# Performance work log

Hardware: AMD Instinct MI355X
Metric: run time of the kernel (lower is better)

The kernel has to match this reference:

```python
import jax, jax.numpy as jnp
import numpy as np

MAX_SEQ_LENGTH = 32
LN_EPS = 1e-5


def setup_inputs() -> dict:
    key = jax.random.key(0)
    ks = jax.random.split(key, 6)
    N, T, D, H, O = 256, 1024, 128, 256, 128
    G = 4 * H
    # torch kaiming_normal_ on a 2D (in, 4H) tensor: fan_in = size(1) = 4H, std = sqrt(2/fan_in)
    std_k = float(np.sqrt(2.0 / G))
    X = jax.random.normal(ks[0], (N, T, D), dtype=jnp.float32)
    Wx = jax.random.normal(ks[1], (D, G), dtype=jnp.float32) * std_k
    Wh = jax.random.normal(ks[2], (H, G), dtype=jnp.float32) * std_k
    b = jnp.zeros((G,), dtype=jnp.float32)
    W1 = jax.random.normal(ks[3], (H, H), dtype=jnp.float32) * float(np.sqrt(1.0 / H))
    b1 = jnp.zeros((H,), dtype=jnp.float32)
    ln_gamma = jnp.ones((H,), dtype=jnp.float32)
    ln_beta = jnp.zeros((H,), dtype=jnp.float32)
    W2 = jax.random.normal(ks[4], (H, O), dtype=jnp.float32) * float(np.sqrt(1.0 / H))
    b2 = jnp.zeros((O,), dtype=jnp.float32)
    return {"X": X, "Wx": Wx, "Wh": Wh, "b": b, "W1": W1, "b1": b1,
            "ln_gamma": ln_gamma, "ln_beta": ln_beta, "W2": W2, "b2": b2}


def _fc(h, W1, b1, ln_gamma, ln_beta, W2, b2):
    z = h @ W1 + b1
    mu = jnp.mean(z, axis=-1, keepdims=True)
    var = jnp.var(z, axis=-1, keepdims=True)
    z = (z - mu) * jax.lax.rsqrt(var + LN_EPS) * ln_gamma + ln_beta
    z = jax.nn.relu(z)
    return z @ W2 + b2


def reference(X, Wx, Wh, b, W1, b1, ln_gamma, ln_beta, W2, b2):
    N, T, D = X.shape
    H = Wh.shape[0]
    h0 = jnp.zeros((N, H), dtype=X.dtype)
    c0 = jnp.zeros((N, H), dtype=X.dtype)

    # --- encoder: standard LSTM cell (sigmoid/tanh gates) ---
    def enc_step(carry, x_t):
        h, c = carry
        fm = x_t @ Wx + h @ Wh + b  # (N, 4H)
        i = jax.nn.sigmoid(fm[:, 0:H])
        f = jax.nn.sigmoid(fm[:, H:2 * H])
        o = jax.nn.sigmoid(fm[:, 2 * H:3 * H])
        g = jnp.tanh(fm[:, 3 * H:4 * H])
        c = c * f + i * g
        h = o * jnp.tanh(c)
        return (h, c), None

    (h, c), _ = jax.lax.scan(enc_step, (h0, c0), jnp.swapaxes(X, 0, 1))

    # --- decoder: NOTE original code uses RAW gate slices (no sigmoid/tanh),
    # and start_token is zeros so the start_token @ Wx term is exactly 0. ---
    def dec_step(carry, _):
        h, c = carry
        fm = h @ Wh + b  # zeros @ Wx contributes 0
        i = fm[:, 0:H]
        f = fm[:, H:2 * H]
        o = fm[:, 2 * H:3 * H]
        g = fm[:, 3 * H:4 * H]
        c = c * f + i * g
        h = o * jnp.tanh(c)
        y = _fc(h, W1, b1, ln_gamma, ln_beta, W2, b2)
        return (h, c), y

    _, ys = jax.lax.scan(dec_step, (h, c), None, length=MAX_SEQ_LENGTH)
    return jnp.swapaxes(ys, 0, 1)  # (N, max_seq_length, output_dim)
```

## Files before the change

kernel.cpp:

```cpp
#include <hip/hip_runtime.h>
#include <cmath>

typedef _Float16 f16;
typedef _Float16 f16x8v __attribute__((ext_vector_type(8)));
typedef float f32x4v __attribute__((ext_vector_type(4)));

#define NTHR 256
#define WPG  16

__device__ __forceinline__ float fexp2_(float x) {
#if __has_builtin(__builtin_amdgcn_exp2f)
  return __builtin_amdgcn_exp2f(x);
#else
  return exp2f(x);
#endif
}
__device__ __forceinline__ float frcp_(float x) {
#if __has_builtin(__builtin_amdgcn_rcpf)
  return __builtin_amdgcn_rcpf(x);
#else
  return 1.0f / x;
#endif
}
__device__ __forceinline__ float fsigmoid(float x) {
  float xc = fminf(fmaxf(x, -60.f), 60.f);
  return frcp_(1.f + fexp2_(xc * -1.44269504f));
}
__device__ __forceinline__ float ftanh_(float x) {
  float xc = fminf(fmaxf(x, -15.f), 15.f);
  float e = fexp2_(xc * 2.88539008f);
  return (e - 1.f) * frcp_(e + 1.f);
}

__device__ __forceinline__ void st_sc_u(unsigned* p, unsigned v) {
  asm volatile("global_store_dword %0, %1, off sc0 sc1" :: "v"(p), "v"(v) : "memory");
}
__device__ __forceinline__ void st_sc_f(float* p, float v) {
  asm volatile("global_store_dword %0, %1, off sc0 sc1" :: "v"(p), "v"(v) : "memory");
}

__device__ __forceinline__ void ld64u_sc(const unsigned* p, uint4& a, uint4& b,
                                         uint4& c, uint4& d) {
  asm volatile(
      "global_load_dwordx4 %0, %4, off sc0 sc1\n\t"
      "global_load_dwordx4 %1, %4, off offset:16 sc0 sc1\n\t"
      "global_load_dwordx4 %2, %4, off offset:32 sc0 sc1\n\t"
      "global_load_dwordx4 %3, %4, off offset:48 sc0 sc1\n\t"
      "s_waitcnt vmcnt(0)"
      : "=&v"(a), "=&v"(b), "=&v"(c), "=&v"(d) : "v"(p) : "memory");
}
__device__ __forceinline__ void ld4f_sc(const float* p, float4& a, float4& b,
                                        float4& c, float4& d) {
  asm volatile(
      "global_load_dwordx4 %0, %4, off sc0 sc1\n\t"
      "global_load_dwordx4 %1, %5, off sc0 sc1\n\t"
      "global_load_dwordx4 %2, %6, off sc0 sc1\n\t"
      "global_load_dwordx4 %3, %7, off sc0 sc1\n\t"
      "s_waitcnt vmcnt(0)"
      : "=&v"(a), "=&v"(b), "=&v"(c), "=&v"(d)
      : "v"(p), "v"(p + 1024), "v"(p + 2048), "v"(p + 3072) : "memory");
}

__device__ __forceinline__ void arrive_bar(unsigned* cg) {
  asm volatile("s_waitcnt vmcnt(0)" ::: "memory");
  __syncthreads();
  if (threadIdx.x == 0)
    (void)__hip_atomic_fetch_add(cg, 1u, __ATOMIC_RELAXED, __HIP_MEMORY_SCOPE_AGENT);
}
__device__ __forceinline__ void wait_bar(unsigned* cg, unsigned target) {
  if (threadIdx.x == 0) {
    unsigned guard = 0;
    while (__hip_atomic_load(cg, __ATOMIC_RELAXED, __HIP_MEMORY_SCOPE_AGENT) < target) {
      __builtin_amdgcn_s_sleep(1);
      if (++guard > (1u << 22)) break;
    }
  }
  __syncthreads();
}

__device__ __forceinline__ unsigned packhl(float v) {
  f16 h = (f16)v;
  f16 lo = (f16)(v - (float)h);
  unsigned short hb, lb;
  __builtin_memcpy(&hb, &h, 2); __builtin_memcpy(&lb, &lo, 2);
  return (unsigned)hb | ((unsigned)lb << 16);
}
__device__ __forceinline__ float unpackf(unsigned u) {
  unsigned short hb = (unsigned short)(u & 0xffffu), lb = (unsigned short)(u >> 16);
  f16 h, l;
  __builtin_memcpy(&h, &hb, 2); __builtin_memcpy(&l, &lb, 2);
  return (float)h + (float)l;
}
__device__ __forceinline__ void unpack_wr(uint4 c, f16* ph, f16* pl) {
  unsigned h01 = (c.x & 0xffffu) | (c.y << 16);
  unsigned h23 = (c.z & 0xffffu) | (c.w << 16);
  unsigned l01 = (c.x >> 16) | (c.y & 0xffff0000u);
  unsigned l23 = (c.z >> 16) | (c.w & 0xffff0000u);
  uint2 hh = {h01, h23}, ll = {l01, l23};
  *(uint2*)ph = hh; *(uint2*)pl = ll;
}
__device__ __forceinline__ void conv8_wr(float4 a, float4 b, f16* ph, f16* pl) {
  f16x8v h, l;
  h[0]=(f16)a.x; h[1]=(f16)a.y; h[2]=(f16)a.z; h[3]=(f16)a.w;
  h[4]=(f16)b.x; h[5]=(f16)b.y; h[6]=(f16)b.z; h[7]=(f16)b.w;
  l[0]=(f16)(a.x-(float)h[0]); l[1]=(f16)(a.y-(float)h[1]);
  l[2]=(f16)(a.z-(float)h[2]); l[3]=(f16)(a.w-(float)h[3]);
  l[4]=(f16)(b.x-(float)h[4]); l[5]=(f16)(b.y-(float)h[5]);
  l[6]=(f16)(b.z-(float)h[6]); l[7]=(f16)(b.w-(float)h[7]);
  *(f16x8v*)ph = h; *(f16x8v*)pl = l;
}

__global__ __launch_bounds__(NTHR, 1) void lstm_k(
    const float* __restrict__ X,  const float* __restrict__ Wx,
    const float* __restrict__ Wh, const float* __restrict__ Bg,
    const float* __restrict__ W1, const float* __restrict__ B1,
    const float* __restrict__ LNG, const float* __restrict__ LNB,
    const float* __restrict__ W2, const float* __restrict__ B2,
    float* __restrict__ Y, unsigned* __restrict__ CNT,
    unsigned* __restrict__ HBp, float* __restrict__ ZB)
{
  __shared__ f16   A_hi[16][392];
  __shared__ f16   A_lo[16][392];
  __shared__ float fm_w[4][16][20];
  __shared__ float hst[16][260];
  __shared__ float w1_lds[16][268];
  __shared__ float w2_lds[8][268];
  __shared__ float lng_lds[256], lnb_lds[256];
  __shared__ float ln_mu[16], ln_rs[16];

  const int tid = threadIdx.x;
  const int wg  = blockIdx.x;
  const int g   = wg & 15;
  const int jm  = wg >> 4;
  const int n0  = g * 16;
  const int k0  = jm * 16;
  unsigned* cg  = CNT + g * 32;

  const int l     = tid & 63;
  const int wv    = __builtin_amdgcn_readfirstlane(tid >> 6);
  const int arow  = l & 15;
  const int krow0 = (l >> 4) * 8;

  const int qq = (l >> 2) & 3;
  const int hc = l & 3;
  const int ch = k0 + 4 * wv + hc;

  f16x8v Bh[12], Bl[12];
  {
    const int bcol = qq * 256 + ch;
    #pragma unroll
    for (int kt = 0; kt < 12; ++kt) {
      #pragma unroll
      for (int j = 0; j < 8; ++j) {
        int k = kt * 32 + krow0 + j;
        float v = (kt < 4) ? Wx[k * 1024 + bcol] : Wh[(k - 128) * 1024 + bcol];
        f16 hi = (f16)v;
        Bh[kt][j] = hi;
        Bl[kt][j] = (f16)(v - (float)hi);
      }
    }
  }

  for (int idx = tid; idx < 256 * 16; idx += NTHR) {
    int k = idx >> 4, cc = idx & 15;
    w1_lds[cc][k] = W1[k * 256 + k0 + cc];
  }
  for (int idx = tid; idx < 256 * 8; idx += NTHR) {
    int k = idx >> 3, cc = idx & 7;
    w2_lds[cc][k] = W2[k * 128 + jm * 8 + cc];
  }
  lng_lds[tid] = LNG[tid];
  lnb_lds[tid] = LNB[tid];

  const float biasI = Bg[        ch];
  const float biasF = Bg[256   + ch];
  const float biasO = Bg[512   + ch];
  const float biasG = Bg[768   + ch];
  const int   myrow = (l >> 4) * 4 + qq;
  float c_reg = 0.0f;

  const int gr = tid >> 4, gk = tid & 15;
  const float b1reg = B1[k0 + gk];
  const float b2reg = (tid < 128) ? B2[jm * 8 + (tid & 7)] : 0.0f;

  {
    const float* xp = X + (size_t)(n0 + (tid >> 4)) * 131072 + (size_t)(tid & 15) * 8;
    conv8_wr(*(const float4*)xp, *(const float4*)(xp + 4),
             &A_hi[tid >> 4][(tid & 15) * 8], &A_lo[tid >> 4][(tid & 15) * 8]);
    f16x8v z8 = {0,0,0,0,0,0,0,0};
    *(f16x8v*)&A_hi[tid >> 4][128 + (tid & 15) * 16]     = z8;
    *(f16x8v*)&A_hi[tid >> 4][128 + (tid & 15) * 16 + 8] = z8;
    *(f16x8v*)&A_lo[tid >> 4][128 + (tid & 15) * 16]     = z8;
    *(f16x8v*)&A_lo[tid >> 4][128 + (tid & 15) * 16 + 8] = z8;
  }
  __syncthreads();

  auto stage_hA = [&](const unsigned* hb) {
    const int row = tid >> 4, cb = (tid & 15) * 16;
    uint4 c0, c1, c2, c3;
    ld64u_sc(hb + (size_t)row * 256 + cb, c0, c1, c2, c3);
    unpack_wr(c0, &A_hi[row][128 + cb],      &A_lo[row][128 + cb]);
    unpack_wr(c1, &A_hi[row][128 + cb + 4],  &A_lo[row][128 + cb + 4]);
    unpack_wr(c2, &A_hi[row][128 + cb + 8],  &A_lo[row][128 + cb + 8]);
    unpack_wr(c3, &A_hi[row][128 + cb + 12], &A_lo[row][128 + cb + 12]);
  };

  for (int t = 0; t < 1024; ++t) {
    float4 xa, xb;
    if (t < 1023) {
      const float* xp = X + (size_t)(n0 + (tid >> 4)) * 131072
                          + (size_t)(t + 1) * 128 + (size_t)(tid & 15) * 8;
      xa = *(const float4*)xp;
      xb = *(const float4*)(xp + 4);
    }

    f32x4v ac0 = {0,0,0,0}, ac1 = {0,0,0,0}, ac2 = {0,0,0,0};
    {
      f16x8v xh[4], xl[4];
      const f16* pah = &A_hi[arow][krow0];
      const f16* pal = &A_lo[arow][krow0];
      #pragma unroll
      for (int kt = 0; kt < 4; ++kt) {
        xh[kt] = *(const f16x8v*)(pah + kt * 32);
        xl[kt] = *(const f16x8v*)(pal + kt * 32);
      }
      #pragma unroll
      for (int kt = 0; kt < 4; ++kt) {
        ac0 = __builtin_amdgcn_mfma_f32_16x16x32_f16(xh[kt], Bh[kt], ac0, 0, 0, 0);
        ac1 = __builtin_amdgcn_mfma_f32_16x16x32_f16(xh[kt], Bl[kt], ac1, 0, 0, 0);
        ac2 = __builtin_amdgcn_mfma_f32_16x16x32_f16(xl[kt], Bh[kt], ac2, 0, 0, 0);
      }
    }

    if (t > 0) {
      wait_bar(cg, (unsigned)(WPG * t));
      stage_hA(HBp + (size_t)((t - 1) & 1) * 65536 + (size_t)n0 * 256);
      __syncthreads();
    }

    {
      f16x8v hh[8], hl[8];
      const f16* pah = &A_hi[arow][128 + krow0];
      const f16* pal = &A_lo[arow][128 + krow0];
      #pragma unroll
      for (int kt = 0; kt < 8; ++kt) {
        hh[kt] = *(const f16x8v*)(pah + kt * 32);
        hl[kt] = *(const f16x8v*)(pal + kt * 32);
      }
      #pragma unroll
      for (int kt = 0; kt < 8; ++kt) {
        ac0 = __builtin_amdgcn_mfma_f32_16x16x32_f16(hh[kt], Bh[kt + 4], ac0, 0, 0, 0);
        ac1 = __builtin_amdgcn_mfma_f32_16x16x32_f16(hh[kt], Bl[kt + 4], ac1, 0, 0, 0);
        ac2 = __builtin_amdgcn_mfma_f32_16x16x32_f16(hl[kt], Bh[kt + 4], ac2, 0, 0, 0);
      }
    }

    {
      f32x4v ac = ac0 + ac1 + ac2;
      *(f32x4v*)&fm_w[wv][l & 15][(l >> 4) * 4] = ac;
      float fi = fm_w[wv][     hc][myrow] + biasI;
      float ff = fm_w[wv][ 4 + hc][myrow] + biasF;
      float fo = fm_w[wv][ 8 + hc][myrow] + biasO;
      float fg = fm_w[wv][12 + hc][myrow] + biasG;
      float si = fsigmoid(fi), sf = fsigmoid(ff), so = fsigmoid(fo);
      float tg = ftanh_(fg);
      c_reg = c_reg * sf + si * tg;
      float hv = so * ftanh_(c_reg);
      st_sc_u(HBp + (size_t)(t & 1) * 65536 + (size_t)(n0 + myrow) * 256 + ch,
              packhl(hv));
    }

    if (t == 0) __syncthreads();
    if (t < 1023)
      conv8_wr(xa, xb, &A_hi[tid >> 4][(tid & 15) * 8], &A_lo[tid >> 4][(tid & 15) * 8]);
    arrive_bar(cg);
  }

  wait_bar(cg, (unsigned)(WPG * 1024));
  stage_hA(HBp + (size_t)65536 + (size_t)n0 * 256);
  __syncthreads();
  unsigned arr = 1024;

  for (int s = 0; s < 32; ++s) {
    const int t = 1024 + s;

    f32x4v ac0 = {0,0,0,0}, ac1 = {0,0,0,0}, ac2 = {0,0,0,0};
    {
      f16x8v hh[8], hl[8];
      const f16* pah = &A_hi[arow][128 + krow0];
      const f16* pal = &A_lo[arow][128 + krow0];
      #pragma unroll
      for (int kt = 0; kt < 8; ++kt) {
        hh[kt] = *(const f16x8v*)(pah + kt * 32);
        hl[kt] = *(const f16x8v*)(pal + kt * 32);
      }
      #pragma unroll
      for (int kt = 0; kt < 8; ++kt) {
        ac0 = __builtin_amdgcn_mfma_f32_16x16x32_f16(hh[kt], Bh[kt + 4], ac0, 0, 0, 0);
        ac1 = __builtin_amdgcn_mfma_f32_16x16x32_f16(hh[kt], Bl[kt + 4], ac1, 0, 0, 0);
        ac2 = __builtin_amdgcn_mfma_f32_16x16x32_f16(hl[kt], Bh[kt + 4], ac2, 0, 0, 0);
      }
    }
    {
      f32x4v ac = ac0 + ac1 + ac2;
      *(f32x4v*)&fm_w[wv][l & 15][(l >> 4) * 4] = ac;
      float fi = fm_w[wv][     hc][myrow] + biasI;
      float ff = fm_w[wv][ 4 + hc][myrow] + biasF;
      float fo = fm_w[wv][ 8 + hc][myrow] + biasO;
      float fg = fm_w[wv][12 + hc][myrow] + biasG;
      c_reg = c_reg * ff + fi * fg;
      float hv = fo * ftanh_(c_reg);
      st_sc_u(HBp + (size_t)(t & 1) * 65536 + (size_t)(n0 + myrow) * 256 + ch,
              packhl(hv));
    }
    arrive_bar(cg); ++arr;
    wait_bar(cg, WPG * arr);

    {
      const int row = tid >> 4, cb = (tid & 15) * 16;
      const unsigned* hb = HBp + (size_t)(t & 1) * 65536 + (size_t)n0 * 256
                               + (size_t)row * 256 + cb;
      uint4 c0, c1, c2, c3;
      ld64u_sc(hb, c0, c1, c2, c3);
      unpack_wr(c0, &A_hi[row][128 + cb],      &A_lo[row][128 + cb]);
      unpack_wr(c1, &A_hi[row][128 + cb + 4],  &A_lo[row][128 + cb + 4]);
      unpack_wr(c2, &A_hi[row][128 + cb + 8],  &A_lo[row][128 + cb + 8]);
      unpack_wr(c3, &A_hi[row][128 + cb + 12], &A_lo[row][128 + cb + 12]);
      float4 f0 = {unpackf(c0.x), unpackf(c0.y), unpackf(c0.z), unpackf(c0.w)};
      float4 f1 = {unpackf(c1.x), unpackf(c1.y), unpackf(c1.z), unpackf(c1.w)};
      float4 f2 = {unpackf(c2.x), unpackf(c2.y), unpackf(c2.z), unpackf(c2.w)};
      float4 f3 = {unpackf(c3.x), unpackf(c3.y), unpackf(c3.z), unpackf(c3.w)};
      *(float4*)&hst[row][cb]      = f0;
      *(float4*)&hst[row][cb + 4]  = f1;
      *(float4*)&hst[row][cb + 8]  = f2;
      *(float4*)&hst[row][cb + 12] = f3;
    }
    __syncthreads();

    {
      float za = b1reg;
      const float* hr = &hst[gr][0];
      const float* wr = &w1_lds[gk][0];
      #pragma unroll 4
      for (int kc = 0; kc < 64; ++kc) {
        float4 h4 = *(const float4*)(hr + kc * 4);
        float4 w4 = *(const float4*)(wr + kc * 4);
        za = fmaf(h4.x, w4.x, fmaf(h4.y, w4.y, fmaf(h4.z, w4.z, fmaf(h4.w, w4.w, za))));
      }
      st_sc_f(ZB + (size_t)(n0 + gr) * 256 + k0 + gk, za);
    }
    arrive_bar(cg); ++arr;
    wait_bar(cg, WPG * arr);

    {
      const float* zs = ZB + (size_t)n0 * 256 + (size_t)tid * 4;
      float4 v0, v1, v2, v3;
      ld4f_sc(zs, v0, v1, v2, v3);
      const int w0 = tid >> 6, cl = (tid & 63) * 4;
      *(float4*)&hst[w0     ][cl] = v0;
      *(float4*)&hst[w0 + 4 ][cl] = v1;
      *(float4*)&hst[w0 + 8 ][cl] = v2;
      *(float4*)&hst[w0 + 12][cl] = v3;
    }
    __syncthreads();

    {
      const float* zr = &hst[gr][0];
      float s1 = 0.f, s2 = 0.f;
      #pragma unroll
      for (int u = 0; u < 16; ++u) { float v = zr[gk * 16 + u]; s1 += v; s2 += v * v; }
      #pragma unroll
      for (int d = 1; d < 16; d <<= 1) { s1 += __shfl_xor(s1, d); s2 += __shfl_xor(s2, d); }
      float mu = s1 * (1.0f / 256.0f);
      float var = s2 * (1.0f / 256.0f) - mu * mu;
      float rstd = rsqrtf(var + 1e-5f);
      if (gk == 0) { ln_mu[gr] = mu; ln_rs[gr] = rstd; }
    }
    __syncthreads();

    #pragma unroll
    for (int rep = 0; rep < 4; ++rep) {
      int f = tid + 256 * rep, r = f >> 6, kq = f & 63;
      float mu = ln_mu[r], rs = ln_rs[r];
      float4 v = *(float4*)&hst[r][kq * 4];
      int cb = kq * 4;
      v.x = fmaxf(fmaf((v.x - mu) * rs, lng_lds[cb    ], lnb_lds[cb    ]), 0.f);
      v.y = fmaxf(fmaf((v.y - mu) * rs, lng_lds[cb + 1], lnb_lds[cb + 1]), 0.f);
      v.z = fmaxf(fmaf((v.z - mu) * rs, lng_lds[cb + 2], lnb_lds[cb + 2]), 0.f);
      v.w = fmaxf(fmaf((v.w - mu) * rs, lng_lds[cb + 3], lnb_lds[cb + 3]), 0.f);
      *(float4*)&hst[r][kq * 4] = v;
    }
    __syncthreads();

    if (tid < 128) {
      int r = tid >> 3, yc = tid & 7;
      float ya = b2reg;
      const float* zr = &hst[r][0];
      const float* wr = &w2_lds[yc][0];
      #pragma unroll 4
      for (int kc = 0; kc < 64; ++kc) {
        float4 z4 = *(const float4*)(zr + kc * 4);
        float4 w4 = *(const float4*)(wr + kc * 4);
        ya = fmaf(z4.x, w4.x, fmaf(z4.y, w4.y, fmaf(z4.z, w4.z, fmaf(z4.w, w4.w, ya))));
      }
      Y[(size_t)(n0 + r) * 4096 + (size_t)s * 128 + jm * 8 + yc] = ya;
    }
    __syncthreads();
  }
}

extern "C" void kernel_launch(void* const* d_in, const int* in_sizes, int n_in,
                              void* d_out, int out_size, void* d_ws, size_t ws_size,
                              hipStream_t stream) {
  const float* X   = (const float*)d_in[0];
  const float* Wx  = (const float*)d_in[1];
  const float* Wh  = (const float*)d_in[2];
  const float* b   = (const float*)d_in[3];
  const float* W1  = (const float*)d_in[4];
  const float* b1  = (const float*)d_in[5];
  const float* lng = (const float*)d_in[6];
  const float* lnb = (const float*)d_in[7];
  const float* W2  = (const float*)d_in[8];
  const float* b2  = (const float*)d_in[9];
  float* Y = (float*)d_out;

  unsigned* CNTp = (unsigned*)d_ws;
  unsigned* HBp  = (unsigned*)((char*)d_ws + 4096);
  float*    ZB   = (float*)((char*)d_ws + 4096 + 524288);
  (void)in_sizes; (void)n_in; (void)out_size; (void)ws_size;

  hipMemsetAsync(d_ws, 0, 2048, stream);
  hipLaunchKernelGGL(lstm_k, dim3(256), dim3(NTHR), 0, stream,
                     X, Wx, Wh, b, W1, b1, lng, lnb, W2, b2, Y, CNTp, HBp, ZB);
}
```

Before: 2.885 ms.

## Replace atomic counter barrier with per-wave flag signaling and parallel polling

Replaces the group-wide atomic fetch-add counter barrier with per-wave monotonic flag slots. Each wave stores its step tag with a coherent store, and one wave per workgroup polls all 64 flags of the group at once using a wave-wide all-reduce. This removes the block-wide __syncthreads before arrival, the atomic contention on a single counter, and the sleep-based spin on the 1024-step encoder critical path. The cost is more polling traffic and a larger flag workspace to zero at launch.

```diff
diff --git a/kernel.cpp b/kernel.cpp
--- a/kernel.cpp
+++ b/kernel.cpp
@@ -38,7 +38,6 @@
 __device__ __forceinline__ void st_sc_f(float* p, float v) {
   asm volatile("global_store_dword %0, %1, off sc0 sc1" :: "v"(p), "v"(v) : "memory");
 }
-
 __device__ __forceinline__ void ld64u_sc(const unsigned* p, uint4& a, uint4& b,
                                          uint4& c, uint4& d) {
   asm volatile(
@@ -61,21 +60,22 @@
       : "v"(p), "v"(p + 1024), "v"(p + 2048), "v"(p + 3072) : "memory");
 }
 
-__device__ __forceinline__ void arrive_bar(unsigned* cg) {
+__device__ __forceinline__ void signal_wave(unsigned* fslot, unsigned tag) {
   asm volatile("s_waitcnt vmcnt(0)" ::: "memory");
-  __syncthreads();
-  if (threadIdx.x == 0)
-    (void)__hip_atomic_fetch_add(cg, 1u, __ATOMIC_RELAXED, __HIP_MEMORY_SCOPE_AGENT);
-}
-__device__ __forceinline__ void wait_bar(unsigned* cg, unsigned target) {
-  if (threadIdx.x == 0) {
-    unsigned guard = 0;
-    while (__hip_atomic_load(cg, __ATOMIC_RELAXED, __HIP_MEMORY_SCOPE_AGENT) < target) {
-      __builtin_amdgcn_s_sleep(1);
-      if (++guard > (1u << 22)) break;
-    }
-  }
-  __syncthreads();
+  if ((threadIdx.x & 63) == 0) st_sc_u(fslot, tag);
+}
+
+__device__ __forceinline__ void poll_flags(const unsigned* fbase, unsigned tag) {
+  const int l = threadIdx.x & 63;
+  const unsigned* p = fbase + (l >> 2) * 16 + (l & 3);
+  unsigned guard = 0;
+  for (;;) {
+    unsigned v;
+    asm volatile("global_load_dword %0, %1, off sc0 sc1\n\ts_waitcnt vmcnt(0)"
+                 : "=v"(v) : "v"(p) : "memory");
+    if (__all((int)(v >= tag))) return;
+    if (++guard > (1u << 22)) return;
+  }
 }
 
 __device__ __forceinline__ unsigned packhl(float v) {
@@ -116,7 +116,8 @@
     const float* __restrict__ W1, const float* __restrict__ B1,
     const float* __restrict__ LNG, const float* __restrict__ LNB,
     const float* __restrict__ W2, const float* __restrict__ B2,
-    float* __restrict__ Y, unsigned* __restrict__ CNT,
+    float* __restrict__ Y,
+    unsigned* __restrict__ FH, unsigned* __restrict__ FZ,
     unsigned* __restrict__ HBp, float* __restrict__ ZB)
 {
   __shared__ f16   A_hi[16][392];
@@ -134,7 +135,8 @@
   const int jm  = wg >> 4;
   const int n0  = g * 16;
   const int k0  = jm * 16;
-  unsigned* cg  = CNT + g * 32;
+  unsigned* FHg = FH + g * 256;
+  unsigned* FZg = FZ + g * 256;
 
   const int l     = tid & 63;
   const int wv    = __builtin_amdgcn_readfirstlane(tid >> 6);
@@ -144,6 +146,8 @@
   const int qq = (l >> 2) & 3;
   const int hc = l & 3;
   const int ch = k0 + 4 * wv + hc;
+  unsigned* myFH = FHg + jm * 16 + wv;
+  unsigned* myFZ = FZg + jm * 16 + wv;
 
   f16x8v Bh[12], Bl[12];
   {
@@ -233,7 +237,8 @@
     }
 
     if (t > 0) {
-      wait_bar(cg, (unsigned)(WPG * t));
+      if (wv == 0) poll_flags(FHg, (unsigned)t);
+      __syncthreads();
       stage_hA(HBp + (size_t)((t - 1) & 1) * 65536 + (size_t)n0 * 256);
       __syncthreads();
     }
@@ -268,18 +273,18 @@
       float hv = so * ftanh_(c_reg);
       st_sc_u(HBp + (size_t)(t & 1) * 65536 + (size_t)(n0 + myrow) * 256 + ch,
               packhl(hv));
-    }
-
-    if (t == 0) __syncthreads();
+      signal_wave(myFH, (unsigned)(t + 1));
+    }
+
     if (t < 1023)
       conv8_wr(xa, xb, &A_hi[tid >> 4][(tid & 15) * 8], &A_lo[tid >> 4][(tid & 15) * 8]);
-    arrive_bar(cg);
-  }
-
-  wait_bar(cg, (unsigned)(WPG * 1024));
+    __syncthreads();
+  }
+
+  if (wv == 0) poll_flags(FHg, 1024u);
+  __syncthreads();
   stage_hA(HBp + (size_t)65536 + (size_t)n0 * 256);
   __syncthreads();
-  unsigned arr = 1024;
 
   for (int s = 0; s < 32; ++s) {
     const int t = 1024 + s;
@@ -312,10 +317,11 @@
       float hv = fo * ftanh_(c_reg);
       st_sc_u(HBp + (size_t)(t & 1) * 65536 + (size_t)(n0 + myrow) * 256 + ch,
               packhl(hv));
-    }
-    arrive_bar(cg); ++arr;
-    wait_bar(cg, WPG * arr);
-
+      signal_wave(myFH, (unsigned)(t + 1));
+    }
+
+    if (wv == 0) poll_flags(FHg, (unsigned)(t + 1));
+    __syncthreads();
     {
       const int row = tid >> 4, cb = (tid & 15) * 16;
       const unsigned* hb = HBp + (size_t)(t & 1) * 65536 + (size_t)n0 * 256
@@ -348,10 +354,11 @@
         za = fmaf(h4.x, w4.x, fmaf(h4.y, w4.y, fmaf(h4.z, w4.z, fmaf(h4.w, w4.w, za))));
       }
       st_sc_f(ZB + (size_t)(n0 + gr) * 256 + k0 + gk, za);
-    }
-    arrive_bar(cg); ++arr;
-    wait_bar(cg, WPG * arr);
-
+      signal_wave(myFZ, (unsigned)(s + 1));
+    }
+
+    if (wv == 0) poll_flags(FZg, (unsigned)(s + 1));
+    __syncthreads();
     {
       const float* zs = ZB + (size_t)n0 * 256 + (size_t)tid * 4;
       float4 v0, v1, v2, v3;
@@ -424,12 +431,13 @@
   const float* b2  = (const float*)d_in[9];
   float* Y = (float*)d_out;
 
-  unsigned* CNTp = (unsigned*)d_ws;
-  unsigned* HBp  = (unsigned*)((char*)d_ws + 4096);
-  float*    ZB   = (float*)((char*)d_ws + 4096 + 524288);
+  unsigned* FH  = (unsigned*)d_ws;
+  unsigned* FZ  = (unsigned*)((char*)d_ws + 16384);
+  unsigned* HBp = (unsigned*)((char*)d_ws + 32768);
+  float*    ZB  = (float*)((char*)d_ws + 32768 + 524288);
   (void)in_sizes; (void)n_in; (void)out_size; (void)ws_size;
 
-  hipMemsetAsync(d_ws, 0, 2048, stream);
+  hipMemsetAsync(d_ws, 0, 32768, stream);
   hipLaunchKernelGGL(lstm_k, dim3(256), dim3(NTHR), 0, stream,
-                     X, Wx, Wh, b, W1, b1, lng, lnb, W2, b2, Y, CNTp, HBp, ZB);
-}
+                     X, Wx, Wh, b, W1, b1, lng, lnb, W2, b2, Y, FH, FZ, HBp, ZB);
+}
```

New measurement: 3.040 ms. +5.4%, slower.
